# Performance work log

Hardware: AMD Instinct MI355X
Metric: run time of the kernel (lower is better)

Reference implementation:

```python
import jax, jax.numpy as jnp
import numpy as np

VOCAB = 50000
D = 512          # in_feat == word_embedding_dim
B = 4096
S = 128
NUM_LABELS = 3


def setup_inputs() -> dict:
    key = jax.random.key(0)
    ks = jax.random.split(key, 16)
    ids_a = jax.random.randint(ks[0], (B, S), 0, VOCAB, dtype=jnp.int32)
    ids_b = jax.random.randint(ks[1], (B, S), 0, VOCAB, dtype=jnp.int32)
    mask_a = jax.random.randint(ks[2], (B, S), 0, 2) > 0
    mask_b = jax.random.randint(ks[3], (B, S), 0, 2) > 0
    s = 0.02
    W_emb = jax.random.normal(ks[4], (VOCAB, D), jnp.float32) * s
    W_emb = W_emb.at[0].set(0.0)  # padding_idx=0
    enc_w1 = jax.random.normal(ks[5], (D, D), jnp.float32) * s
    enc_b1 = jnp.zeros((D,), jnp.float32)
    enc_w2 = jax.random.normal(ks[6], (D, D), jnp.float32) * s
    enc_b2 = jnp.zeros((D,), jnp.float32)
    cls_w1 = jax.random.normal(ks[7], (2 * D, D), jnp.float32) * s
    cls_b1 = jnp.zeros((D,), jnp.float32)
    cls_w2 = jax.random.normal(ks[8], (D, NUM_LABELS), jnp.float32) * s
    cls_b2 = jnp.zeros((NUM_LABELS,), jnp.float32)
    return {
        "text_a_inputs_id": ids_a, "text_b_inputs_id": ids_b,
        "text_a_attention_mask": mask_a, "text_b_attention_mask": mask_b,
        "W_emb": W_emb,
        "enc_w1": enc_w1, "enc_b1": enc_b1, "enc_w2": enc_w2, "enc_b2": enc_b2,
        "cls_w1": cls_w1, "cls_b1": cls_b1, "cls_w2": cls_w2, "cls_b2": cls_b2,
    }


def _encode(ids, mask, W_emb, w1, b1, w2, b2):
    # embedding gather [B,S,D], fused masked sum-pool -> [B,D]
    emb = W_emb[ids]
    pooled = jnp.einsum("bsd,bs->bd", emb, mask.astype(emb.dtype))
    x = jnp.tanh(pooled @ w1 + b1)
    x = jnp.tanh(x @ w2 + b2)  # dropout is identity in eval
    return x


def reference(text_a_inputs_id, text_b_inputs_id, text_a_attention_mask,
              text_b_attention_mask, W_emb, enc_w1, enc_b1, enc_w2, enc_b2,
              cls_w1, cls_b1, cls_w2, cls_b2):
    va = _encode(text_a_inputs_id, text_a_attention_mask, W_emb, enc_w1, enc_b1, enc_w2, enc_b2)
    vb = _encode(text_b_inputs_id, text_b_attention_mask, W_emb, enc_w1, enc_b1, enc_w2, enc_b2)
    pooled = jnp.concatenate([va, vb], axis=-1)  # [B, 2D]
    h = jnp.tanh(pooled @ cls_w1 + cls_b1)
    logits = h @ cls_w2 + cls_b2  # [B, num_labels]
    return logits
```

## Files before the change

kernel.cpp:

```cpp
#include <hip/hip_runtime.h>


typedef unsigned short u16;
typedef __attribute__((ext_vector_type(8))) short short8;
typedef __attribute__((ext_vector_type(4))) float f32x4;

__device__ __forceinline__ float bfu2f(u16 u) {
    union { unsigned int i; float f; } v;
    v.i = ((unsigned int)u) << 16;
    return v.f;
}

__device__ __forceinline__ u16 f2bfu(float f) {
    union { float f; unsigned int i; } v;
    v.f = f;
    unsigned int x = v.i;
    x += 0x7fffu + ((x >> 16) & 1u);
    return (u16)(x >> 16);
}

__device__ __forceinline__ float fast_tanh(float x) {
    float xc = fminf(fmaxf(x, -15.f), 15.f);
    float e = __builtin_amdgcn_exp2f(xc * 2.885390082f);
    return (e - 1.f) / (e + 1.f);
}

__device__ __forceinline__ int detect_wave(const u16* __restrict__ W,
                                           const unsigned int* __restrict__ m,
                                           int lane)
{
    int cnt = 0;
    int w01 = 1, b01 = 1, lo16 = 0;
    #pragma unroll
    for (int j = lane; j < 256; j += 64) {
        u16 u = W[1024 + 2 * j];
        int e = (u >> 7) & 0xFF;
        cnt += (e >= 0x6A && e <= 0x7E) ? 1 : 0;
        unsigned int v = m[j];
        w01 &= (v <= 1u) ? 1 : 0;
        b01 &= ((v & ~0x01010101u) == 0u) ? 1 : 0;
        lo16 |= ((v & 0xFFFFu) == 0x3F80u) ? 1 : 0;
    }
    #pragma unroll
    for (int off = 32; off > 0; off >>= 1) {
        cnt  += __shfl_down(cnt, off);
        w01  &= __shfl_down(w01, off);
        b01  &= __shfl_down(b01, off);
        lo16 |= __shfl_down(lo16, off);
    }
    int mtype;
    if (w01)        mtype = 0;
    else if (b01)   mtype = 1;
    else if (lo16)  mtype = 2;
    else            mtype = 3;
    int fl = ((cnt >= 128) ? 1 : 0) | (mtype << 2);
    return __shfl(fl, 0);
}

__device__ __forceinline__ int mask_nonzero(const void* __restrict__ msk,
                                            int idx, int mtype)
{
    switch (mtype) {
        case 0:  return ((const int*)msk)[idx] != 0;
        case 1:  return ((const unsigned char*)msk)[idx] != 0;
        case 2:  return ((const u16*)msk)[idx] != 0;
        default: return ((const unsigned int*)msk)[idx] != 0u;
    }
}

__global__ __launch_bounds__(128) void pool_kernel(
    const int* __restrict__ ids, const void* __restrict__ msk,
    const void* __restrict__ W, u16* __restrict__ P,
    const unsigned int* __restrict__ Mdet)
{
    __shared__ int s_ids[128];
    __shared__ int s_cnt;
    __shared__ int s_flags;
    __shared__ float sP[512];
    const int t = threadIdx.x;
    const int w = t >> 6;
    const int lane = t & 63;

    if (t == 0) s_cnt = 0;
    if (t < 64) {
        int fl = detect_wave((const u16*)W, Mdet, t);
        if (t == 0) s_flags = fl;
    }
    __syncthreads();
    const int  flags = s_flags;
    const bool isbf  = (flags & 1) != 0;
    const int  mtype = (flags >> 2) & 3;

    const int row = blockIdx.x;

    int id = ids[row * 128 + t];
    int mk = mask_nonzero(msk, row * 128 + t, mtype);
    if (mk) {
        int idx = atomicAdd(&s_cnt, 1);
        s_ids[idx] = id;
    }
    __syncthreads();
    const int cnt = s_cnt;

    float acc[8] = {};
    if (isbf) {
        const u16* Wb = (const u16*)W;
        int j = w;
        for (; j + 6 < cnt; j += 8) {
            union { uint4 v; u16 s[8]; } r0, r1, r2, r3;
            r0.v = *(const uint4*)(Wb + (size_t)s_ids[j + 0] * 512 + lane * 8);
            r1.v = *(const uint4*)(Wb + (size_t)s_ids[j + 2] * 512 + lane * 8);
            r2.v = *(const uint4*)(Wb + (size_t)s_ids[j + 4] * 512 + lane * 8);
            r3.v = *(const uint4*)(Wb + (size_t)s_ids[j + 6] * 512 + lane * 8);
            #pragma unroll
            for (int i = 0; i < 8; ++i)
                acc[i] += bfu2f(r0.s[i]) + bfu2f(r1.s[i]) +
                          bfu2f(r2.s[i]) + bfu2f(r3.s[i]);
        }
        for (; j < cnt; j += 2) {
            union { uint4 v; u16 s[8]; } r;
            r.v = *(const uint4*)(Wb + (size_t)s_ids[j] * 512 + lane * 8);
            #pragma unroll
            for (int i = 0; i < 8; ++i) acc[i] += bfu2f(r.s[i]);
        }
    } else {
        const float* Wf = (const float*)W;
        for (int j = w; j < cnt; j += 2) {
            const float* rp = Wf + (size_t)s_ids[j] * 512 + lane * 8;
            float4 a = *(const float4*)(rp + 0);
            float4 b = *(const float4*)(rp + 4);
            acc[0] += a.x; acc[1] += a.y; acc[2] += a.z; acc[3] += a.w;
            acc[4] += b.x; acc[5] += b.y; acc[6] += b.z; acc[7] += b.w;
        }
    }

    if (w == 0) {
        #pragma unroll
        for (int i = 0; i < 8; ++i) sP[lane * 8 + i] = acc[i];
    }
    __syncthreads();
    if (w == 1) {
        union { uint4 v; u16 s[8]; } o;
        #pragma unroll
        for (int i = 0; i < 8; ++i)
            o.s[i] = f2bfu(acc[i] + sP[lane * 8 + i]);
        *(uint4*)(P + (size_t)row * 512 + lane * 8) = o.v;
    }
}

template<bool ISBF>
__device__ __forceinline__ void gemm_body(
    const u16* __restrict__ A, const u16* __restrict__ A2, int K1,
    const void* __restrict__ Bv, const void* __restrict__ biasv,
    u16* __restrict__ C, int N, int K,
    u16* __restrict__ As, u16* __restrict__ Bs)
{
    const int tid  = threadIdx.x;
    const int lane = tid & 63;
    const int wid = tid >> 6;
    const int wm  = (wid & 1) * 64;
    const int wn  = (wid >> 1) * 32;
    const int ar = tid >> 2;
    const int ak = (tid & 3) * 8;
    const int bk = tid >> 3;
    const int jn = tid & 7;
    const int nb = jn * 8;
    const int bofs = (((bk >> 3) + jn) & 3) * 8 + (bk & 7);
    const int lm = lane & 15;
    const int kq = lane >> 4;
    const int kc = kq * 8;
    const int m0 = blockIdx.x * 128;
    const int n0 = blockIdx.y * 64;

    const u16*   Bb = (const u16*)Bv;
    const float* Bf = (const float*)Bv;

    f32x4 acc[4][2];
    #pragma unroll
    for (int i = 0; i < 4; ++i)
        #pragma unroll
        for (int j = 0; j < 2; ++j)
            acc[i][j] = (f32x4){0.f, 0.f, 0.f, 0.f};

    uint4 ra0, ra1;
    uint4 rbb;
    float4 rf0, rf1;

    #define FETCH(k0)                                                         \
    {                                                                         \
        const int kg = (k0) + ak;                                             \
        const u16* base = (kg < K1) ? (A + kg) : (A2 + (kg - K1));            \
        ra0 = *(const uint4*)(base + (size_t)(m0 + ar) * 512);                \
        ra1 = *(const uint4*)(base + (size_t)(m0 + ar + 64) * 512);           \
        if constexpr (ISBF) {                                                 \
            rbb = *(const uint4*)(Bb + (size_t)((k0) + bk) * N + n0 + nb);    \
        } else {                                                              \
            const float* Bp = Bf + (size_t)((k0) + bk) * N + n0 + nb;         \
            rf0 = *(const float4*)(Bp + 0);                                   \
            rf1 = *(const float4*)(Bp + 4);                                   \
        }                                                                     \
    }

    FETCH(0)
    for (int k0 = 0; k0 < K; k0 += 32) {
        if (k0) __syncthreads();
        *(uint4*)&As[ar * 40 + ak]        = ra0;
        *(uint4*)&As[(ar + 64) * 40 + ak] = ra1;
        u16 bvals[8];
        if constexpr (ISBF) {
            union { uint4 v; u16 s[8]; } ub; ub.v = rbb;
            #pragma unroll
            for (int i = 0; i < 8; ++i) bvals[i] = ub.s[i];
        } else {
            bvals[0] = f2bfu(rf0.x); bvals[1] = f2bfu(rf0.y);
            bvals[2] = f2bfu(rf0.z); bvals[3] = f2bfu(rf0.w);
            bvals[4] = f2bfu(rf1.x); bvals[5] = f2bfu(rf1.y);
            bvals[6] = f2bfu(rf1.z); bvals[7] = f2bfu(rf1.w);
        }
        #pragma unroll
        for (int i = 0; i < 8; ++i)
            Bs[(nb + i) * 40 + bofs] = bvals[i];
        __syncthreads();

        if (k0 + 32 < K) FETCH(k0 + 32)

        short8 af[4], bf[2];
        #pragma unroll
        for (int i = 0; i < 4; ++i)
            af[i] = *(const short8*)&As[(wm + i * 16 + lm) * 40 + kc];
        #pragma unroll
        for (int j = 0; j < 2; ++j) {
            const int n = wn + j * 16 + lm;
            const int ch = ((kq + (n >> 3)) & 3) * 8;
            bf[j] = *(const short8*)&Bs[n * 40 + ch];
        }
        #pragma unroll
        for (int i = 0; i < 4; ++i)
            #pragma unroll
            for (int j = 0; j < 2; ++j)
                acc[i][j] = __builtin_amdgcn_mfma_f32_16x16x32_bf16(
                    af[i], bf[j], acc[i][j], 0, 0, 0);
    }
    #undef FETCH

    #pragma unroll
    for (int j = 0; j < 2; ++j) {
        const int n = n0 + wn + j * 16 + lm;
        const float bsv = ISBF ? bfu2f(((const u16*)biasv)[n])
                               : ((const float*)biasv)[n];
        #pragma unroll
        for (int i = 0; i < 4; ++i) {
            #pragma unroll
            for (int r = 0; r < 4; ++r) {
                const int m = m0 + wm + i * 16 + kq * 4 + r;
                C[(size_t)m * N + n] = f2bfu(fast_tanh(acc[i][j][r] + bsv));
            }
        }
    }
}

__global__ __launch_bounds__(256, 2) void gemm_mfma(
    const u16* __restrict__ A, const u16* __restrict__ A2, int K1,
    const void* __restrict__ B, const void* __restrict__ bias,
    u16* __restrict__ C, int N, int K,
    const u16* __restrict__ Wdet, const unsigned int* __restrict__ Mdet)
{
    __shared__ __align__(16) u16 As[128 * 40];
    __shared__ __align__(16) u16 Bs[64 * 40];
    __shared__ int s_flags;

    if (threadIdx.x < 64) {
        int fl = detect_wave(Wdet, Mdet, threadIdx.x);
        if (threadIdx.x == 0) s_flags = fl;
    }
    __syncthreads();
    if (s_flags & 1) gemm_body<true >(A, A2, K1, B, bias, C, N, K, As, Bs);
    else             gemm_body<false>(A, A2, K1, B, bias, C, N, K, As, Bs);
}

__global__ __launch_bounds__(64) void logits_kernel(
    const u16* __restrict__ H, const void* __restrict__ W2,
    const void* __restrict__ b2, float* __restrict__ out,
    const u16* __restrict__ Wdet, const unsigned int* __restrict__ Mdet)
{
    const int lane = threadIdx.x;
    const int fl = detect_wave(Wdet, Mdet, lane);
    const bool isbf = (fl & 1) != 0;

    const int m = blockIdx.x;
    union { uint4 v; u16 s[8]; } h;
    h.v = *(const uint4*)(H + (size_t)m * 512 + lane * 8);

    float a0 = 0.f, a1 = 0.f, a2 = 0.f;
    #pragma unroll
    for (int i = 0; i < 8; ++i) {
        const int k = lane * 8 + i;
        float x = bfu2f(h.s[i]);
        float w0, w1, w2;
        if (isbf) {
            const u16* Wb = (const u16*)W2;
            w0 = bfu2f(Wb[k * 3 + 0]); w1 = bfu2f(Wb[k * 3 + 1]); w2 = bfu2f(Wb[k * 3 + 2]);
        } else {
            const float* Wf = (const float*)W2;
            w0 = Wf[k * 3 + 0]; w1 = Wf[k * 3 + 1]; w2 = Wf[k * 3 + 2];
        }
        a0 += x * w0; a1 += x * w1; a2 += x * w2;
    }
    #pragma unroll
    for (int off = 32; off > 0; off >>= 1) {
        a0 += __shfl_down(a0, off);
        a1 += __shfl_down(a1, off);
        a2 += __shfl_down(a2, off);
    }
    if (lane == 0) {
        float b0, b1, b2v;
        if (isbf) {
            const u16* bb = (const u16*)b2;
            b0 = bfu2f(bb[0]); b1 = bfu2f(bb[1]); b2v = bfu2f(bb[2]);
        } else {
            const float* bf = (const float*)b2;
            b0 = bf[0]; b1 = bf[1]; b2v = bf[2];
        }
        out[m * 3 + 0] = a0 + b0;
        out[m * 3 + 1] = a1 + b1;
        out[m * 3 + 2] = a2 + b2v;
    }
}

extern "C" void kernel_launch(void* const* d_in, const int* in_sizes, int n_in,
                              void* d_out, int out_size, void* d_ws, size_t ws_size,
                              hipStream_t stream)
{
    const int* ids_a  = (const int*)d_in[0];
    const int* ids_b  = (const int*)d_in[1];
    const void* mask_a = d_in[2];
    const void* mask_b = d_in[3];
    const void* W_emb  = d_in[4];
    const void* enc_w1 = d_in[5];
    const void* enc_b1 = d_in[6];
    const void* enc_w2 = d_in[7];
    const void* enc_b2 = d_in[8];
    const void* cls_w1 = d_in[9];
    const void* cls_b1 = d_in[10];
    const void* cls_w2 = d_in[11];
    const void* cls_b2 = d_in[12];

    const u16* Wdet = (const u16*)W_emb;
    const unsigned int* Mdet = (const unsigned int*)mask_a;

    u16* buf0 = (u16*)d_ws;
    u16* buf1 = buf0 + (size_t)8192 * 512;

    pool_kernel<<<4096, 128, 0, stream>>>(ids_a, mask_a, W_emb, buf0, Mdet);
    pool_kernel<<<4096, 128, 0, stream>>>(ids_b, mask_b, W_emb,
                                          buf0 + (size_t)4096 * 512, Mdet);

    gemm_mfma<<<dim3(64, 8), 256, 0, stream>>>(
        buf0, buf0, 512, enc_w1, enc_b1, buf1, 512, 512, Wdet, Mdet);

    gemm_mfma<<<dim3(64, 8), 256, 0, stream>>>(
        buf1, buf1, 512, enc_w2, enc_b2, buf0, 512, 512, Wdet, Mdet);

    gemm_mfma<<<dim3(32, 8), 256, 0, stream>>>(
        buf0, buf0 + (size_t)4096 * 512, 512, cls_w1, cls_b1, buf1, 512, 1024, Wdet, Mdet);

    logits_kernel<<<4096, 64, 0, stream>>>(buf1, cls_w2, cls_b2, (float*)d_out, Wdet, Mdet);
}
```

Before: 376.1 us.

## Double-buffer GEMM LDS with 512-thread blocks and merge pool launches

The GEMM kernel now uses 8 waves per block, each computing a 32x32 sub-tile, and double-buffers the A/B shared-memory tiles so it needs only one barrier per k-step. The two pool launches are merged into one grid of 8192 blocks that selects the a or b inputs by block index. This aims to improve latency hiding and occupancy in the GEMMs and to remove one launch. In exchange it uses twice the LDS per block and does less MFMA work per wave relative to its LDS reads.

```diff
diff --git a/kernel.cpp b/kernel.cpp
--- a/kernel.cpp
+++ b/kernel.cpp
@@ -69,7 +69,8 @@
 }
 
 __global__ __launch_bounds__(128) void pool_kernel(
-    const int* __restrict__ ids, const void* __restrict__ msk,
+    const int* __restrict__ ids_a, const int* __restrict__ ids_b,
+    const void* __restrict__ mska, const void* __restrict__ mskb,
     const void* __restrict__ W, u16* __restrict__ P,
     const unsigned int* __restrict__ Mdet)
 {
@@ -92,9 +93,12 @@
     const int  mtype = (flags >> 2) & 3;
 
     const int row = blockIdx.x;
-
-    int id = ids[row * 128 + t];
-    int mk = mask_nonzero(msk, row * 128 + t, mtype);
+    const int r   = row & 4095;
+    const int* __restrict__ ids = (row < 4096) ? ids_a : ids_b;
+    const void* __restrict__ msk = (row < 4096) ? mska : mskb;
+
+    int id = ids[r * 128 + t];
+    int mk = mask_nonzero(msk, r * 128 + t, mtype);
     if (mk) {
         int idx = atomicAdd(&s_cnt, 1);
         s_ids[idx] = id;
@@ -118,10 +122,10 @@
                           bfu2f(r2.s[i]) + bfu2f(r3.s[i]);
         }
         for (; j < cnt; j += 2) {
-            union { uint4 v; u16 s[8]; } r;
-            r.v = *(const uint4*)(Wb + (size_t)s_ids[j] * 512 + lane * 8);
+            union { uint4 v; u16 s[8]; } rr;
+            rr.v = *(const uint4*)(Wb + (size_t)s_ids[j] * 512 + lane * 8);
             #pragma unroll
-            for (int i = 0; i < 8; ++i) acc[i] += bfu2f(r.s[i]);
+            for (int i = 0; i < 8; ++i) acc[i] += bfu2f(rr.s[i]);
         }
     } else {
         const float* Wf = (const float*)W;
@@ -153,13 +157,13 @@
     const u16* __restrict__ A, const u16* __restrict__ A2, int K1,
     const void* __restrict__ Bv, const void* __restrict__ biasv,
     u16* __restrict__ C, int N, int K,
-    u16* __restrict__ As, u16* __restrict__ Bs)
+    u16* __restrict__ As0, u16* __restrict__ Bs0)
 {
     const int tid  = threadIdx.x;
     const int lane = tid & 63;
     const int wid = tid >> 6;
-    const int wm  = (wid & 1) * 64;
-    const int wn  = (wid >> 1) * 32;
+    const int wm  = (wid & 3) * 32;
+    const int wn  = (wid >> 2) * 32;
     const int ar = tid >> 2;
     const int ak = (tid & 3) * 8;
     const int bk = tid >> 3;
@@ -175,14 +179,14 @@
     const u16*   Bb = (const u16*)Bv;
     const float* Bf = (const float*)Bv;
 
-    f32x4 acc[4][2];
-    #pragma unroll
-    for (int i = 0; i < 4; ++i)
+    f32x4 acc[2][2];
+    #pragma unroll
+    for (int i = 0; i < 2; ++i)
         #pragma unroll
         for (int j = 0; j < 2; ++j)
             acc[i][j] = (f32x4){0.f, 0.f, 0.f, 0.f};
 
-    uint4 ra0, ra1;
+    uint4 ra;
     uint4 rbb;
     float4 rf0, rf1;
 
@@ -190,58 +194,75 @@
     {                                                                         \
         const int kg = (k0) + ak;                                             \
         const u16* base = (kg < K1) ? (A + kg) : (A2 + (kg - K1));            \
-        ra0 = *(const uint4*)(base + (size_t)(m0 + ar) * 512);                \
-        ra1 = *(const uint4*)(base + (size_t)(m0 + ar + 64) * 512);           \
-        if constexpr (ISBF) {                                                 \
-            rbb = *(const uint4*)(Bb + (size_t)((k0) + bk) * N + n0 + nb);    \
-        } else {                                                              \
-            const float* Bp = Bf + (size_t)((k0) + bk) * N + n0 + nb;         \
-            rf0 = *(const float4*)(Bp + 0);                                   \
-            rf1 = *(const float4*)(Bp + 4);                                   \
+        ra = *(const uint4*)(base + (size_t)(m0 + ar) * 512);                 \
+        if (tid < 256) {                                                      \
+            if constexpr (ISBF) {                                             \
+                rbb = *(const uint4*)(Bb + (size_t)((k0) + bk) * N + n0 + nb);\
+            } else {                                                          \
+                const float* Bp = Bf + (size_t)((k0) + bk) * N + n0 + nb;     \
+                rf0 = *(const float4*)(Bp + 0);                               \
+                rf1 = *(const float4*)(Bp + 4);                               \
+            }                                                                 \
         }                                                                     \
     }
 
+    #define STORE(pp)                                                         \
+    {                                                                         \
+        *(uint4*)&As0[(pp) * 5120 + ar * 40 + ak] = ra;                       \
+        if (tid < 256) {                                                      \
+            u16 bvals[8];                                                     \
+            if constexpr (ISBF) {                                             \
+                union { uint4 v; u16 s[8]; } ub; ub.v = rbb;                  \
+                _Pragma("unroll")                                             \
+                for (int i = 0; i < 8; ++i) bvals[i] = ub.s[i];               \
+            } else {                                                          \
+                bvals[0] = f2bfu(rf0.x); bvals[1] = f2bfu(rf0.y);             \
+                bvals[2] = f2bfu(rf0.z); bvals[3] = f2bfu(rf0.w);             \
+                bvals[4] = f2bfu(rf1.x); bvals[5] = f2bfu(rf1.y);             \
+                bvals[6] = f2bfu(rf1.z); bvals[7] = f2bfu(rf1.w);             \
+            }                                                                 \
+            _Pragma("unroll")                                                 \
+            for (int i = 0; i < 8; ++i)                                       \
+                Bs0[(pp) * 2560 + (nb + i) * 40 + bofs] = bvals[i];           \
+        }                                                                     \
+    }
+
     FETCH(0)
+    STORE(0)
+    FETCH(32)
+    __syncthreads();
+
+    int p = 0;
     for (int k0 = 0; k0 < K; k0 += 32) {
-        if (k0) __syncthreads();
-        *(uint4*)&As[ar * 40 + ak]        = ra0;
-        *(uint4*)&As[(ar + 64) * 40 + ak] = ra1;
-        u16 bvals[8];
-        if constexpr (ISBF) {
-            union { uint4 v; u16 s[8]; } ub; ub.v = rbb;
-            #pragma unroll
-            for (int i = 0; i < 8; ++i) bvals[i] = ub.s[i];
-        } else {
-            bvals[0] = f2bfu(rf0.x); bvals[1] = f2bfu(rf0.y);
-            bvals[2] = f2bfu(rf0.z); bvals[3] = f2bfu(rf0.w);
-            bvals[4] = f2bfu(rf1.x); bvals[5] = f2bfu(rf1.y);
-            bvals[6] = f2bfu(rf1.z); bvals[7] = f2bfu(rf1.w);
-        }
-        #pragma unroll
-        for (int i = 0; i < 8; ++i)
-            Bs[(nb + i) * 40 + bofs] = bvals[i];
-        __syncthreads();
-
-        if (k0 + 32 < K) FETCH(k0 + 32)
-
-        short8 af[4], bf[2];
-        #pragma unroll
-        for (int i = 0; i < 4; ++i)
-            af[i] = *(const short8*)&As[(wm + i * 16 + lm) * 40 + kc];
+        if (k0 + 32 < K) {
+            STORE(p ^ 1)
+            if (k0 + 64 < K) FETCH(k0 + 64)
+        }
+
+        const u16* Ap = As0 + p * 5120;
+        const u16* Bp2 = Bs0 + p * 2560;
+        short8 af[2], bf[2];
+        #pragma unroll
+        for (int i = 0; i < 2; ++i)
+            af[i] = *(const short8*)&Ap[(wm + i * 16 + lm) * 40 + kc];
         #pragma unroll
         for (int j = 0; j < 2; ++j) {
             const int n = wn + j * 16 + lm;
             const int ch = ((kq + (n >> 3)) & 3) * 8;
-            bf[j] = *(const short8*)&Bs[n * 40 + ch];
-        }
-        #pragma unroll
-        for (int i = 0; i < 4; ++i)
+            bf[j] = *(const short8*)&Bp2[n * 40 + ch];
+        }
+        #pragma unroll
+        for (int i = 0; i < 2; ++i)
             #pragma unroll
             for (int j = 0; j < 2; ++j)
                 acc[i][j] = __builtin_amdgcn_mfma_f32_16x16x32_bf16(
                     af[i], bf[j], acc[i][j], 0, 0, 0);
+
+        if (k0 + 32 < K) __syncthreads();
+        p ^= 1;
     }
     #undef FETCH
+    #undef STORE
 
     #pragma unroll
     for (int j = 0; j < 2; ++j) {
@@ -249,7 +270,7 @@
         const float bsv = ISBF ? bfu2f(((const u16*)biasv)[n])
                                : ((const float*)biasv)[n];
         #pragma unroll
-        for (int i = 0; i < 4; ++i) {
+        for (int i = 0; i < 2; ++i) {
             #pragma unroll
             for (int r = 0; r < 4; ++r) {
                 const int m = m0 + wm + i * 16 + kq * 4 + r;
@@ -259,14 +280,14 @@
     }
 }
 
-__global__ __launch_bounds__(256, 2) void gemm_mfma(
+__global__ __launch_bounds__(512, 4) void gemm_mfma(
     const u16* __restrict__ A, const u16* __restrict__ A2, int K1,
     const void* __restrict__ B, const void* __restrict__ bias,
     u16* __restrict__ C, int N, int K,
     const u16* __restrict__ Wdet, const unsigned int* __restrict__ Mdet)
 {
-    __shared__ __align__(16) u16 As[128 * 40];
-    __shared__ __align__(16) u16 Bs[64 * 40];
+    __shared__ __align__(16) u16 As[2 * 128 * 40];
+    __shared__ __align__(16) u16 Bs[2 * 64 * 40];
     __shared__ int s_flags;
 
     if (threadIdx.x < 64) {
@@ -351,17 +372,16 @@
     u16* buf0 = (u16*)d_ws;
     u16* buf1 = buf0 + (size_t)8192 * 512;
 
-    pool_kernel<<<4096, 128, 0, stream>>>(ids_a, mask_a, W_emb, buf0, Mdet);
-    pool_kernel<<<4096, 128, 0, stream>>>(ids_b, mask_b, W_emb,
-                                          buf0 + (size_t)4096 * 512, Mdet);
-
-    gemm_mfma<<<dim3(64, 8), 256, 0, stream>>>(
+    pool_kernel<<<8192, 128, 0, stream>>>(ids_a, ids_b, mask_a, mask_b,
+                                          W_emb, buf0, Mdet);
+
+    gemm_mfma<<<dim3(64, 8), 512, 0, stream>>>(
         buf0, buf0, 512, enc_w1, enc_b1, buf1, 512, 512, Wdet, Mdet);
 
-    gemm_mfma<<<dim3(64, 8), 256, 0, stream>>>(
+    gemm_mfma<<<dim3(64, 8), 512, 0, stream>>>(
         buf1, buf1, 512, enc_w2, enc_b2, buf0, 512, 512, Wdet, Mdet);
 
-    gemm_mfma<<<dim3(32, 8), 256, 0, stream>>>(
+    gemm_mfma<<<dim3(32, 8), 512, 0, stream>>>(
         buf0, buf0 + (size_t)4096 * 512, 512, cls_w1, cls_b1, buf1, 512, 1024, Wdet, Mdet);
 
     logits_kernel<<<4096, 64, 0, stream>>>(buf1, cls_w2, cls_b2, (float*)d_out, Wdet, Mdet);
```

Result: faster. 357.4 us (-5.0%).
